# Kernel tuning notes

Hardware: AMD Instinct MI355X
Metric: run time of the kernel (lower is better)

## Reference

```python
import jax, jax.numpy as jnp
import numpy as np

L, V, D, H, F, S = 6, 32000, 768, 12, 3072, 1024
B, T = 2, 1024
DK = D // H
EPS = 1e-5  # torch LayerNorm default


def _ln(x, w, b):
    m = x.mean(-1, keepdims=True)
    v = ((x - m) ** 2).mean(-1, keepdims=True)
    return (x - m) / jnp.sqrt(v + EPS) * w + b


def setup_inputs() -> dict:
    key = jax.random.key(0)
    ks = jax.random.split(key, 16)
    n = lambda k, shape: jax.random.normal(k, shape, jnp.float32) * 0.02
    return {
        "x": jax.random.randint(ks[0], (B, T), 0, V),
        "tok_emb": n(ks[1], (V, D)),
        "pos_emb": n(ks[2], (S, D)),
        "ln1_w": jnp.ones((L, D), jnp.float32), "ln1_b": jnp.zeros((L, D), jnp.float32),
        "wq": n(ks[3], (L, D, D)), "bq": jnp.zeros((L, D), jnp.float32),
        "wk": n(ks[4], (L, D, D)), "bk": jnp.zeros((L, D), jnp.float32),
        "wv": n(ks[5], (L, D, D)), "bv": jnp.zeros((L, D), jnp.float32),
        "wo": n(ks[6], (L, D, D)), "bo": jnp.zeros((L, D), jnp.float32),
        "ln2_w": jnp.ones((L, D), jnp.float32), "ln2_b": jnp.zeros((L, D), jnp.float32),
        "w1": n(ks[7], (L, F, D)), "b1": jnp.zeros((L, F), jnp.float32),
        "w2": n(ks[8], (L, D, F)), "b2": jnp.zeros((L, D), jnp.float32),
        "lnf_w": jnp.ones((D,), jnp.float32), "lnf_b": jnp.zeros((D,), jnp.float32),
        "head_w": n(ks[9], (V, D)),
    }


def reference(x, tok_emb, pos_emb, ln1_w, ln1_b, wq, bq, wk, bk, wv, bv, wo, bo,
              ln2_w, ln2_b, w1, b1, w2, b2, lnf_w, lnf_b, head_w):
    Bx, Tx = x.shape
    h = tok_emb[x] + pos_emb[:Tx]                     # [B,T,D]
    causal = jnp.triu(jnp.ones((Tx, Tx), bool), 1)    # True above diagonal
    scale = 1.0 / np.sqrt(DK)
    for i in range(L):
        a = _ln(h, ln1_w[i], ln1_b[i])
        q = (a @ wq[i].T + bq[i]).reshape(Bx, Tx, H, DK).transpose(0, 2, 1, 3)
        k = (a @ wk[i].T + bk[i]).reshape(Bx, Tx, H, DK).transpose(0, 2, 1, 3)
        v = (a @ wv[i].T + bv[i]).reshape(Bx, Tx, H, DK).transpose(0, 2, 1, 3)
        scores = jnp.einsum("bhtd,bhsd->bhts", q, k) * scale  # [B,H,T,T]
        scores = jnp.where(causal, -jnp.inf, scores)
        attn = jax.nn.softmax(scores, axis=-1)
        ctx = jnp.einsum("bhts,bhsd->bhtd", attn, v)
        ctx = ctx.transpose(0, 2, 1, 3).reshape(Bx, Tx, D)
        h = h + ctx @ wo[i].T + bo[i]
        f = _ln(h, ln2_w[i], ln2_b[i])
        h = h + jax.nn.relu(f @ w1[i].T + b1[i]) @ w2[i].T + b2[i]
    h = _ln(h, lnf_w, lnf_b)
    return h @ head_w.T                               # [B,T,V] logits
```

## Files before the change

### kernel.cpp

```cpp
#include <hip/hip_runtime.h>

typedef unsigned short u16;
typedef __bf16 bf16x8 __attribute__((ext_vector_type(8)));
typedef float f32x4 __attribute__((ext_vector_type(4)));
typedef float f32x4v __attribute__((ext_vector_type(4)));
typedef u16 u16x4 __attribute__((ext_vector_type(4)));

__device__ __forceinline__ float bf2f(u16 u) {
    unsigned x = ((unsigned)u) << 16;
    return __builtin_bit_cast(float, x);
}
__device__ __forceinline__ u16 f2bf(float f) {
    unsigned x = __builtin_bit_cast(unsigned, f);
    unsigned r = (x + 0x7FFFu + ((x >> 16) & 1u)) >> 16;
    return (u16)r;
}

__global__ __launch_bounds__(256) void cvt_kernel(const float* __restrict__ in,
                                                  u16* __restrict__ out, long n) {
    for (long i = (long)blockIdx.x * 1024 + (long)threadIdx.x * 4; i < n;
         i += (long)gridDim.x * 1024) {
        f32x4v v = *(const f32x4v*)(in + i);
        u16x4 o;
        o.x = f2bf(v.x); o.y = f2bf(v.y); o.z = f2bf(v.z); o.w = f2bf(v.w);
        *(u16x4*)(out + i) = o;
    }
}

__global__ __launch_bounds__(256) void bias_fuse_kernel(const float* __restrict__ bq,
                                                        const float* __restrict__ bk,
                                                        const float* __restrict__ bv,
                                                        float* __restrict__ dst) {
    int i = blockIdx.x * 256 + threadIdx.x;
    if (i < 6 * 768) {
        int l = i / 768, j = i % 768;
        dst[l * 2304 + j] = bq[i];
        dst[l * 2304 + 768 + j] = bk[i];
        dst[l * 2304 + 1536 + j] = bv[i];
    }
}

__global__ __launch_bounds__(256) void embed_kernel(const int* __restrict__ x,
                                                    const float* __restrict__ tok,
                                                    const float* __restrict__ pos,
                                                    float* __restrict__ h) {
    int row = blockIdx.x;
    int t = row & 1023;
    long id = x[row];
    const float* te = tok + id * 768L;
    const float* pe = pos + (long)t * 768L;
    float* o = h + (long)row * 768L;
    for (int d = threadIdx.x; d < 768; d += 256) o[d] = te[d] + pe[d];
}

__global__ __launch_bounds__(256) void ln_kernel(const float* __restrict__ x,
                                                 const float* __restrict__ w,
                                                 const float* __restrict__ b,
                                                 u16* __restrict__ out) {
    __shared__ float red[4];
    int row = blockIdx.x;
    const float* xr = x + (long)row * 768L;
    int tid = threadIdx.x, lane = tid & 63, wid = tid >> 6;
    float v0 = xr[tid], v1 = xr[tid + 256], v2 = xr[tid + 512];
    float s = v0 + v1 + v2;
    for (int o = 32; o; o >>= 1) s += __shfl_xor(s, o);
    if (lane == 0) red[wid] = s;
    __syncthreads();
    float mean = (red[0] + red[1] + red[2] + red[3]) * (1.f / 768.f);
    __syncthreads();
    float d0 = v0 - mean, d1 = v1 - mean, d2 = v2 - mean;
    float q = d0 * d0 + d1 * d1 + d2 * d2;
    for (int o = 32; o; o >>= 1) q += __shfl_xor(q, o);
    if (lane == 0) red[wid] = q;
    __syncthreads();
    float var = (red[0] + red[1] + red[2] + red[3]) * (1.f / 768.f);
    float rstd = rsqrtf(var + 1e-5f);
    u16* orow = out + (long)row * 768L;
    orow[tid]       = f2bf(d0 * rstd * w[tid]       + b[tid]);
    orow[tid + 256] = f2bf(d1 * rstd * w[tid + 256] + b[tid + 256]);
    orow[tid + 512] = f2bf(d2 * rstd * w[tid + 512] + b[tid + 512]);
}

__global__ __launch_bounds__(256) void redln_kernel(
    const float* __restrict__ part, long pstride, int S,
    const float* __restrict__ bias, float* __restrict__ h,
    const float* __restrict__ w, const float* __restrict__ b,
    u16* __restrict__ out) {
    __shared__ float red[4];
    int row = blockIdx.x;
    int tid = threadIdx.x, lane = tid & 63, wid = tid >> 6;
    long base = (long)row * 768;
    float v[3];
#pragma unroll
    for (int e3 = 0; e3 < 3; e3++) {
        int e = tid + 256 * e3;
        float x = h[base + e] + bias[e];
        for (int s = 0; s < S; s++) x += part[(long)s * pstride + base + e];
        v[e3] = x;
        h[base + e] = x;
    }
    float s = v[0] + v[1] + v[2];
    for (int o = 32; o; o >>= 1) s += __shfl_xor(s, o);
    if (lane == 0) red[wid] = s;
    __syncthreads();
    float mean = (red[0] + red[1] + red[2] + red[3]) * (1.f / 768.f);
    __syncthreads();
    float d0 = v[0] - mean, d1 = v[1] - mean, d2 = v[2] - mean;
    float q = d0 * d0 + d1 * d1 + d2 * d2;
    for (int o = 32; o; o >>= 1) q += __shfl_xor(q, o);
    if (lane == 0) red[wid] = q;
    __syncthreads();
    float var = (red[0] + red[1] + red[2] + red[3]) * (1.f / 768.f);
    float rstd = rsqrtf(var + 1e-5f);
    u16* orow = out + base;
    orow[tid]       = f2bf(d0 * rstd * w[tid]       + b[tid]);
    orow[tid + 256] = f2bf(d1 * rstd * w[tid + 256] + b[tid + 256]);
    orow[tid + 512] = f2bf(d2 * rstd * w[tid + 512] + b[tid + 512]);
}

__global__ __launch_bounds__(256) void flash_kernel(
    const u16* __restrict__ qkv,
    const u16* __restrict__ vT,
    u16* __restrict__ ctx) {
    int z = blockIdx.z;
    int zb = z / 12, zh = z - zb * 12;
    int qt = (int)gridDim.x - 1 - (int)blockIdx.x;
    int q0 = qt * 64;
    int tid = threadIdx.x, lane = tid & 63, wid = tid >> 6;
    int rA = lane & 15, sA = lane >> 4;

    const u16* Qbase = qkv + (long)zb * 1024 * 2304 + zh * 64;
    const u16* Kbase = Qbase + 768;
    const u16* Vbase = vT + (long)z * 64 * 1024;

    __shared__ u16 Ks[64 * 64];
    __shared__ u16 Vs[64 * 64];
    __shared__ u16 Ps[4][16 * 64];

    bf16x8 aq[2];
    {
        const u16* qrow = Qbase + (long)(q0 + wid * 16 + rA) * 2304;
        aq[0] = *(const bf16x8*)(qrow + sA * 8);
        aq[1] = *(const bf16x8*)(qrow + 32 + sA * 8);
    }

    float m[4], l[4];
    f32x4 acc_o[4];
#pragma unroll
    for (int j = 0; j < 4; j++) { m[j] = -1e30f; l[j] = 0.f; }
#pragma unroll
    for (int nf = 0; nf < 4; nf++) acc_o[nf] = 0.f;

    int grow0 = q0 + wid * 16 + sA * 4;
    int nkv = qt + 1;
    for (int t = 0; t < nkv; ++t) {
        int kv0 = t * 64;
#pragma unroll
        for (int c0 = 0; c0 < 512; c0 += 256) {
            int c = c0 + tid;
            int row = c >> 3, half = (c >> 2) & 1, sl = c & 3;
            int ks = sl ^ ((row >> 1) & 3);
            __builtin_amdgcn_global_load_lds(
                (const __attribute__((address_space(1))) unsigned*)(Kbase + (long)(kv0 + row) * 2304 + half * 32 + ks * 8),
                (__attribute__((address_space(3))) unsigned*)(Ks + c * 8), 16, 0, 0);
        }
#pragma unroll
        for (int c0 = 0; c0 < 512; c0 += 256) {
            int c = c0 + tid;
            int row = c >> 3, half = (c >> 2) & 1, sl = c & 3;
            int ks = sl ^ ((row >> 1) & 3);
            __builtin_amdgcn_global_load_lds(
                (const __attribute__((address_space(1))) unsigned*)(Vbase + (long)row * 1024 + kv0 + half * 32 + ks * 8),
                (__attribute__((address_space(3))) unsigned*)(Vs + c * 8), 16, 0, 0);
        }
        __syncthreads();

        f32x4 s[4];
#pragma unroll
        for (int nf = 0; nf < 4; nf++) s[nf] = 0.f;
#pragma unroll
        for (int h = 0; h < 2; h++)
#pragma unroll
            for (int nf = 0; nf < 4; nf++) {
                int row = nf * 16 + rA;
                bf16x8 bk_ = *(const bf16x8*)(Ks + row * 64 + h * 32 + ((sA ^ ((row >> 1) & 3))) * 8);
                s[nf] = __builtin_amdgcn_mfma_f32_16x16x32_bf16(aq[h], bk_, s[nf], 0, 0, 0);
            }
#pragma unroll
        for (int nf = 0; nf < 4; nf++) {
            int col = kv0 + nf * 16 + rA;
#pragma unroll
            for (int j = 0; j < 4; j++)
                s[nf][j] = (col <= grow0 + j) ? s[nf][j] * 0.125f : -1e30f;
        }
        float pm[4];
#pragma unroll
        for (int j = 0; j < 4; j++) {
            float v = fmaxf(fmaxf(s[0][j], s[1][j]), fmaxf(s[2][j], s[3][j]));
#pragma unroll
            for (int o = 1; o < 16; o <<= 1) v = fmaxf(v, __shfl_xor(v, o));
            pm[j] = v;
        }
        float esc[4];
#pragma unroll
        for (int j = 0; j < 4; j++) {
            float mn = fmaxf(m[j], pm[j]);
            esc[j] = __expf(m[j] - mn);
            m[j] = mn;
        }
        float ts[4] = {0.f, 0.f, 0.f, 0.f};
#pragma unroll
        for (int nf = 0; nf < 4; nf++) {
            int c = nf * 16 + rA;
            int half = c >> 5, ch = (c >> 3) & 3, e = c & 7;
#pragma unroll
            for (int j = 0; j < 4; j++) {
                float p = __expf(s[nf][j] - m[j]);
                ts[j] += p;
                int r = sA * 4 + j;
                Ps[wid][r * 64 + half * 32 + (ch ^ ((r >> 1) & 3)) * 8 + e] = f2bf(p);
            }
        }
#pragma unroll
        for (int j = 0; j < 4; j++) {
            float v = ts[j];
#pragma unroll
            for (int o = 1; o < 16; o <<= 1) v += __shfl_xor(v, o);
            l[j] = l[j] * esc[j] + v;
        }
#pragma unroll
        for (int nf = 0; nf < 4; nf++)
#pragma unroll
            for (int j = 0; j < 4; j++) acc_o[nf][j] *= esc[j];

#pragma unroll
        for (int h = 0; h < 2; h++) {
            bf16x8 ap = *(const bf16x8*)(Ps[wid] + rA * 64 + h * 32 + ((sA ^ ((rA >> 1) & 3))) * 8);
#pragma unroll
            for (int nf = 0; nf < 4; nf++) {
                int row = nf * 16 + rA;
                bf16x8 bv_ = *(const bf16x8*)(Vs + row * 64 + h * 32 + ((sA ^ ((row >> 1) & 3))) * 8);
                acc_o[nf] = __builtin_amdgcn_mfma_f32_16x16x32_bf16(ap, bv_, acc_o[nf], 0, 0, 0);
            }
        }
        __syncthreads();
    }

    float inv[4];
#pragma unroll
    for (int j = 0; j < 4; j++) inv[j] = 1.f / l[j];
    u16* crow = ctx + ((long)zb * 1024 + q0 + wid * 16) * 768 + zh * 64;
#pragma unroll
    for (int nf = 0; nf < 4; nf++)
#pragma unroll
        for (int j = 0; j < 4; j++)
            crow[(long)(sA * 4 + j) * 768 + nf * 16 + rA] = f2bf(acc_o[nf][j] * inv[j]);
}

template <int BM, int BN, int EPI, int SK>
__global__ __launch_bounds__(256) void gemm3_kernel(
    const u16* __restrict__ A, int lda,
    const u16* __restrict__ Bm, int ldb,
    void* __restrict__ Cv, int ldc,
    const float* __restrict__ bias, int Kslice, int gm,
    u16* __restrict__ aux, int gemmBlocks, long partStride,
    const float* __restrict__ c0src, u16* __restrict__ c0dst, long c0n,
    const float* __restrict__ c1src, u16* __restrict__ c1dst, long c1n) {
    constexpr int BK = 32;
    int flat = blockIdx.x;
    int tid = threadIdx.x;
    if (flat >= gemmBlocks) {
        int P = (int)gridDim.x - gemmBlocks;
        int pid = flat - gemmBlocks;
        int P0 = P >> 1;
        const float* src; u16* dst; long n; long b0; long nb;
        if (pid < P0) { src = c0src; dst = c0dst; n = c0n; b0 = pid; nb = P0; }
        else { src = c1src; dst = c1dst; n = c1n; b0 = pid - P0; nb = P - P0; }
        if (src) {
            for (long i = b0 * 1024 + (long)tid * 4; i < n; i += nb * 1024) {
                f32x4v v = *(const f32x4v*)(src + i);
                u16x4 o;
                o.x = f2bf(v.x); o.y = f2bf(v.y); o.z = f2bf(v.z); o.w = f2bf(v.w);
                *(u16x4*)(dst + i) = o;
            }
        }
        return;
    }
    int nwg = gemmBlocks;
    int qq = nwg >> 3, rr = nwg & 7;
    int xcd = flat & 7, wi = flat >> 3;
    int swz = (xcd < rr) ? (xcd * (qq + 1) + wi) : (rr * (qq + 1) + (xcd - rr) * qq + wi);
    int slice = 0, wblk = swz;
    if (SK > 1) { int nbs = nwg / SK; slice = swz / nbs; wblk = swz - slice * nbs; }
    int ntile = wblk / gm, mt = wblk - ntile * gm;
    int bm0 = mt * BM, bn0 = ntile * BN;
    long koff = (long)slice * Kslice;
    const u16* Ab = A + (long)bm0 * lda + koff;
    const u16* Bb = Bm + (long)bn0 * ldb + koff;

    __shared__ u16 As[2][BM * BK];
    __shared__ u16 Bs[2][BN * BK];

    int lane = tid & 63, wid = tid >> 6;
    constexpr int WM = BM / 2, WN = BN / 2, MR = WM / 16, NR = WN / 16;
    int wm0 = (wid >> 1) * WM, wn0 = (wid & 1) * WN;

    f32x4 acc[MR][NR];
#pragma unroll
    for (int mi = 0; mi < MR; mi++)
#pragma unroll
        for (int ni = 0; ni < NR; ni++) acc[mi][ni] = 0.f;

    int nt = Kslice / BK;

    auto stage = [&](int buf, int k0) {
        constexpr int CA = BM * 4;
#pragma unroll
        for (int c0 = 0; c0 < CA; c0 += 256) {
            int c = c0 + tid;
            int row = c >> 2, sl = c & 3;
            int ks = sl ^ ((row >> 1) & 3);
            __builtin_amdgcn_global_load_lds(
                (const __attribute__((address_space(1))) unsigned*)(Ab + (long)row * lda + k0 + ks * 8),
                (__attribute__((address_space(3))) unsigned*)(As[buf] + c * 8), 16, 0, 0);
        }
        constexpr int CB = BN * 4;
#pragma unroll
        for (int c0 = 0; c0 < CB; c0 += 256) {
            int c = c0 + tid;
            int row = c >> 2, sl = c & 3;
            int ks = sl ^ ((row >> 1) & 3);
            __builtin_amdgcn_global_load_lds(
                (const __attribute__((address_space(1))) unsigned*)(Bb + (long)row * ldb + k0 + ks * 8),
                (__attribute__((address_space(3))) unsigned*)(Bs[buf] + c * 8), 16, 0, 0);
        }
    };

    stage(0, 0);
    __syncthreads();
    int cur = 0;
    int rA = lane & 15, sA = lane >> 4;
    int sswz = (sA ^ ((rA >> 1) & 3)) * 8;
    for (int t = 0; t < nt; ++t) {
        if (t + 1 < nt) stage(cur ^ 1, (t + 1) * BK);
        bf16x8 af[MR], bfr[NR];
#pragma unroll
        for (int mi = 0; mi < MR; mi++)
            af[mi] = *(const bf16x8*)(As[cur] + (wm0 + mi * 16 + rA) * BK + sswz);
#pragma unroll
        for (int ni = 0; ni < NR; ni++)
            bfr[ni] = *(const bf16x8*)(Bs[cur] + (wn0 + ni * 16 + rA) * BK + sswz);
#pragma unroll
        for (int mi = 0; mi < MR; mi++)
#pragma unroll
            for (int ni = 0; ni < NR; ni++)
                acc[mi][ni] = __builtin_amdgcn_mfma_f32_16x16x32_bf16(
                    af[mi], bfr[ni], acc[mi][ni], 0, 0, 0);
        __syncthreads();
        cur ^= 1;
    }

#pragma unroll
    for (int mi = 0; mi < MR; mi++)
#pragma unroll
        for (int ni = 0; ni < NR; ni++) {
            int gmb = bm0 + wm0 + mi * 16 + ((lane >> 4) << 2);
            int gn = bn0 + wn0 + ni * 16 + (lane & 15);
            if (EPI == 6) {
                if (gn < 1536) {
#pragma unroll
                    for (int j = 0; j < 4; j++)
                        ((u16*)Cv)[(long)(gmb + j) * ldc + gn] =
                            f2bf(acc[mi][ni][j] + bias[gn]);
                } else {
                    u16x4 o;
#pragma unroll
                    for (int j = 0; j < 4; j++) o[j] = f2bf(acc[mi][ni][j] + bias[gn]);
                    int hh = (gn - 1536) >> 6, dk = gn & 63;
                    long off = ((long)((gmb >> 10) * 12 + hh) * 64 + dk) * 1024 + (gmb & 1023);
                    *(u16x4*)(aux + off) = o;
                }
            } else {
#pragma unroll
                for (int j = 0; j < 4; j++) {
                    float v = acc[mi][ni][j];
                    long idx = (long)(gmb + j) * ldc + gn;
                    if (EPI == 2) ((u16*)Cv)[idx] = f2bf(fmaxf(v + bias[gn], 0.f));
                    else ((float*)Cv)[(long)slice * partStride + idx] = v;
                }
            }
        }
}

extern "C" void kernel_launch(void* const* d_in, const int* in_sizes, int n_in,
                              void* d_out, int out_size, void* d_ws, size_t ws_size,
                              hipStream_t stream) {
    const int L = 6, D = 768, F = 3072, T = 1024, V = 32000;
    const int M = 2048;
    const int* x = (const int*)d_in[0];
    const float* tok = (const float*)d_in[1];
    const float* pos = (const float*)d_in[2];
    const float* ln1w = (const float*)d_in[3];
    const float* ln1b = (const float*)d_in[4];
    const float* wq = (const float*)d_in[5];
    const float* bq = (const float*)d_in[6];
    const float* wk = (const float*)d_in[7];
    const float* bk = (const float*)d_in[8];
    const float* wv = (const float*)d_in[9];
    const float* bv = (const float*)d_in[10];
    const float* wo = (const float*)d_in[11];
    const float* bo = (const float*)d_in[12];
    const float* ln2w = (const float*)d_in[13];
    const float* ln2b = (const float*)d_in[14];
    const float* w1 = (const float*)d_in[15];
    const float* b1 = (const float*)d_in[16];
    const float* w2 = (const float*)d_in[17];
    const float* b2 = (const float*)d_in[18];
    const float* lnfw = (const float*)d_in[19];
    const float* lnfb = (const float*)d_in[20];
    const float* headw = (const float*)d_in[21];

    char* p = (char*)d_ws;
    auto alloc = [&](size_t bytes) {
        char* r = p;
        p += (bytes + 255) & ~(size_t)255;
        return r;
    };
    const long DD = (long)D * D, FD = (long)F * D;
    const long PS = (long)M * D;
    const long HC = 2048000;
    u16* qkvw_b = (u16*)alloc(L * 3 * DD * 2);
    u16* wo_b = (u16*)alloc(L * DD * 2);
    u16* w1_b = (u16*)alloc(L * FD * 2);
    u16* w2_b = (u16*)alloc(L * FD * 2);
    u16* hw_b = (u16*)alloc((long)V * D * 2);
    float* qkvbias = (float*)alloc(L * 2304 * 4);
    float* h = (float*)alloc((long)M * D * 4);
    u16* a = (u16*)alloc((long)M * D * 2);
    u16* qkvb = (u16*)alloc((long)M * 2304 * 2);
    u16* vT = (u16*)alloc(24L * 64 * T * 2);
    u16* ctxb = (u16*)alloc((long)M * D * 2);
    u16* f1 = (u16*)alloc((long)M * F * 2);
    float* part = (float*)alloc(4L * PS * 4);

    auto cvt = [&](const float* src, u16* dst, long n) {
        long blocks = (n + 1023) / 1024;
        if (blocks > 4096) blocks = 4096;
        cvt_kernel<<<dim3((unsigned)blocks), 256, 0, stream>>>(src, dst, n);
    };
    cvt(wq, qkvw_b, DD);
    cvt(wk, qkvw_b + DD, DD);
    cvt(wv, qkvw_b + 2 * DD, DD);
    cvt(wo, wo_b, DD);
    cvt(w1, w1_b, FD);
    cvt(w2, w2_b, FD);
    bias_fuse_kernel<<<dim3(18), 256, 0, stream>>>(bq, bk, bv, qkvbias);
    embed_kernel<<<dim3(M), 256, 0, stream>>>(x, tok, pos, h);
    ln_kernel<<<dim3(M), 256, 0, stream>>>(h, ln1w, ln1b, a);

    for (int i = 0; i < L; i++) {
        int nx = i + 1;
        bool hn = nx < L;
        {
            int pg = hn ? 128 : 0;
            gemm3_kernel<128, 128, 6, 1><<<dim3(288 + pg), 256, 0, stream>>>(
                a, D, qkvw_b + i * 3 * DD, D, qkvb, 2304, qkvbias + i * 2304,
                D, 16, vT, 288, 0,
                hn ? wq + nx * DD : nullptr, qkvw_b + nx * 3 * DD, DD,
                hn ? wk + nx * DD : nullptr, qkvw_b + nx * 3 * DD + DD, DD);
        }
        flash_kernel<<<dim3(16, 1, 24), 256, 0, stream>>>(qkvb, vT, ctxb);
        gemm3_kernel<64, 128, 5, 2><<<dim3(384 + 128), 256, 0, stream>>>(
            ctxb, D, wo_b + i * DD, D, part, D, nullptr, 384, 32, nullptr,
            384, PS,
            hn ? wv + nx * DD : nullptr, qkvw_b + nx * 3 * DD + 2 * DD, DD,
            hn ? wo + nx * DD : nullptr, wo_b + nx * DD, DD);
        redln_kernel<<<dim3(M), 256, 0, stream>>>(
            part, PS, 2, bo + i * D, h, ln2w + i * D, ln2b + i * D, a);
        gemm3_kernel<128, 128, 2, 1><<<dim3(384 + 128), 256, 0, stream>>>(
            a, D, w1_b + i * FD, D, f1, F, b1 + i * F, D, 16, nullptr, 384, 0,
            hn ? w1 + nx * FD : nullptr, w1_b + nx * FD, FD,
            headw + (2 * i) * HC, hw_b + (2 * i) * HC, HC);
        gemm3_kernel<64, 128, 5, 4><<<dim3(768 + 128), 256, 0, stream>>>(
            f1, F, w2_b + i * FD, F, part, D, nullptr, 768, 32, nullptr,
            768, PS,
            hn ? w2 + nx * FD : nullptr, w2_b + nx * FD, FD,
            headw + (2 * i + 1) * HC, hw_b + (2 * i + 1) * HC, HC);
        redln_kernel<<<dim3(M), 256, 0, stream>>>(
            part, PS, 4, b2 + i * D, h,
            hn ? ln1w + nx * D : lnfw, hn ? ln1b + nx * D : lnfb, a);
    }
    gemm3_kernel<128, 128, 5, 1><<<dim3(4000), 256, 0, stream>>>(
        a, D, hw_b, D, d_out, V, nullptr, D, 16, nullptr, 4000, 0,
        nullptr, nullptr, 0, nullptr, nullptr, 0);
}
```

Measured before the change: 1.114 ms.

## Load GEMM fragments directly from global into registers instead of LDS staging

Drops the LDS double-buffered staging in the GEMM kernel. Each wave now loads its MFMA fragments straight from global memory into registers, with a two-deep register prefetch, and the per-tile __syncthreads is removed. This cuts the LDS round trip and the barriers, but gives up sharing data between waves, so each operand row is fetched by several waves (relying on L1/L2) and the global loads are less coalesced. The fp32-to-bf16 conversion loops also process 8 elements per thread instead of 4.

```diff
diff --git a/kernel.cpp b/kernel.cpp
--- a/kernel.cpp
+++ b/kernel.cpp
@@ -18,12 +18,15 @@
 
 __global__ __launch_bounds__(256) void cvt_kernel(const float* __restrict__ in,
                                                   u16* __restrict__ out, long n) {
-    for (long i = (long)blockIdx.x * 1024 + (long)threadIdx.x * 4; i < n;
-         i += (long)gridDim.x * 1024) {
-        f32x4v v = *(const f32x4v*)(in + i);
-        u16x4 o;
-        o.x = f2bf(v.x); o.y = f2bf(v.y); o.z = f2bf(v.z); o.w = f2bf(v.w);
-        *(u16x4*)(out + i) = o;
+    for (long i = (long)blockIdx.x * 2048 + (long)threadIdx.x * 8; i < n;
+         i += (long)gridDim.x * 2048) {
+        f32x4v v0 = *(const f32x4v*)(in + i);
+        f32x4v v1 = *(const f32x4v*)(in + i + 4);
+        u16x4 o0, o1;
+        o0.x = f2bf(v0.x); o0.y = f2bf(v0.y); o0.z = f2bf(v0.z); o0.w = f2bf(v0.w);
+        o1.x = f2bf(v1.x); o1.y = f2bf(v1.y); o1.z = f2bf(v1.z); o1.w = f2bf(v1.w);
+        *(u16x4*)(out + i) = o0;
+        *(u16x4*)(out + i + 4) = o1;
     }
 }
 
@@ -258,7 +261,7 @@
 }
 
 template <int BM, int BN, int EPI, int SK>
-__global__ __launch_bounds__(256) void gemm3_kernel(
+__global__ __launch_bounds__(256) void gemm6_kernel(
     const u16* __restrict__ A, int lda,
     const u16* __restrict__ Bm, int ldb,
     void* __restrict__ Cv, int ldc,
@@ -277,11 +280,14 @@
         if (pid < P0) { src = c0src; dst = c0dst; n = c0n; b0 = pid; nb = P0; }
         else { src = c1src; dst = c1dst; n = c1n; b0 = pid - P0; nb = P - P0; }
         if (src) {
-            for (long i = b0 * 1024 + (long)tid * 4; i < n; i += nb * 1024) {
-                f32x4v v = *(const f32x4v*)(src + i);
-                u16x4 o;
-                o.x = f2bf(v.x); o.y = f2bf(v.y); o.z = f2bf(v.z); o.w = f2bf(v.w);
-                *(u16x4*)(dst + i) = o;
+            for (long i = b0 * 2048 + (long)tid * 8; i < n; i += nb * 2048) {
+                f32x4v v0 = *(const f32x4v*)(src + i);
+                f32x4v v1 = *(const f32x4v*)(src + i + 4);
+                u16x4 o0, o1;
+                o0.x = f2bf(v0.x); o0.y = f2bf(v0.y); o0.z = f2bf(v0.z); o0.w = f2bf(v0.w);
+                o1.x = f2bf(v1.x); o1.y = f2bf(v1.y); o1.z = f2bf(v1.z); o1.w = f2bf(v1.w);
+                *(u16x4*)(dst + i) = o0;
+                *(u16x4*)(dst + i + 4) = o1;
             }
         }
         return;
@@ -295,15 +301,20 @@
     int ntile = wblk / gm, mt = wblk - ntile * gm;
     int bm0 = mt * BM, bn0 = ntile * BN;
     long koff = (long)slice * Kslice;
-    const u16* Ab = A + (long)bm0 * lda + koff;
-    const u16* Bb = Bm + (long)bn0 * ldb + koff;
-
-    __shared__ u16 As[2][BM * BK];
-    __shared__ u16 Bs[2][BN * BK];
 
     int lane = tid & 63, wid = tid >> 6;
     constexpr int WM = BM / 2, WN = BN / 2, MR = WM / 16, NR = WN / 16;
     int wm0 = (wid >> 1) * WM, wn0 = (wid & 1) * WN;
+    int rA = lane & 15, sA = lane >> 4;
+
+    const u16* ap[MR];
+    const u16* bp[NR];
+#pragma unroll
+    for (int mi = 0; mi < MR; mi++)
+        ap[mi] = A + (long)(bm0 + wm0 + mi * 16 + rA) * lda + koff + sA * 8;
+#pragma unroll
+    for (int ni = 0; ni < NR; ni++)
+        bp[ni] = Bm + (long)(bn0 + wn0 + ni * 16 + rA) * ldb + koff + sA * 8;
 
     f32x4 acc[MR][NR];
 #pragma unroll
@@ -313,51 +324,36 @@
 
     int nt = Kslice / BK;
 
-    auto stage = [&](int buf, int k0) {
-        constexpr int CA = BM * 4;
-#pragma unroll
-        for (int c0 = 0; c0 < CA; c0 += 256) {
-            int c = c0 + tid;
-            int row = c >> 2, sl = c & 3;
-            int ks = sl ^ ((row >> 1) & 3);
-            __builtin_amdgcn_global_load_lds(
-                (const __attribute__((address_space(1))) unsigned*)(Ab + (long)row * lda + k0 + ks * 8),
-                (__attribute__((address_space(3))) unsigned*)(As[buf] + c * 8), 16, 0, 0);
-        }
-        constexpr int CB = BN * 4;
-#pragma unroll
-        for (int c0 = 0; c0 < CB; c0 += 256) {
-            int c = c0 + tid;
-            int row = c >> 2, sl = c & 3;
-            int ks = sl ^ ((row >> 1) & 3);
-            __builtin_amdgcn_global_load_lds(
-                (const __attribute__((address_space(1))) unsigned*)(Bb + (long)row * ldb + k0 + ks * 8),
-                (__attribute__((address_space(3))) unsigned*)(Bs[buf] + c * 8), 16, 0, 0);
-        }
-    };
-
-    stage(0, 0);
-    __syncthreads();
-    int cur = 0;
-    int rA = lane & 15, sA = lane >> 4;
-    int sswz = (sA ^ ((rA >> 1) & 3)) * 8;
-    for (int t = 0; t < nt; ++t) {
-        if (t + 1 < nt) stage(cur ^ 1, (t + 1) * BK);
-        bf16x8 af[MR], bfr[NR];
-#pragma unroll
-        for (int mi = 0; mi < MR; mi++)
-            af[mi] = *(const bf16x8*)(As[cur] + (wm0 + mi * 16 + rA) * BK + sswz);
-#pragma unroll
-        for (int ni = 0; ni < NR; ni++)
-            bfr[ni] = *(const bf16x8*)(Bs[cur] + (wn0 + ni * 16 + rA) * BK + sswz);
+    bf16x8 a0[MR], b0[NR], a1[MR], b1[NR];
+#pragma unroll
+    for (int mi = 0; mi < MR; mi++) a0[mi] = *(const bf16x8*)(ap[mi]);
+#pragma unroll
+    for (int ni = 0; ni < NR; ni++) b0[ni] = *(const bf16x8*)(bp[ni]);
+
+    for (int i = 0; i < nt / 2; ++i) {
+        int t1 = 2 * i + 1, t2 = 2 * i + 2;
+#pragma unroll
+        for (int mi = 0; mi < MR; mi++) a1[mi] = *(const bf16x8*)(ap[mi] + t1 * BK);
+#pragma unroll
+        for (int ni = 0; ni < NR; ni++) b1[ni] = *(const bf16x8*)(bp[ni] + t1 * BK);
 #pragma unroll
         for (int mi = 0; mi < MR; mi++)
 #pragma unroll
             for (int ni = 0; ni < NR; ni++)
                 acc[mi][ni] = __builtin_amdgcn_mfma_f32_16x16x32_bf16(
-                    af[mi], bfr[ni], acc[mi][ni], 0, 0, 0);
-        __syncthreads();
-        cur ^= 1;
+                    a0[mi], b0[ni], acc[mi][ni], 0, 0, 0);
+        if (t2 < nt) {
+#pragma unroll
+            for (int mi = 0; mi < MR; mi++) a0[mi] = *(const bf16x8*)(ap[mi] + t2 * BK);
+#pragma unroll
+            for (int ni = 0; ni < NR; ni++) b0[ni] = *(const bf16x8*)(bp[ni] + t2 * BK);
+        }
+#pragma unroll
+        for (int mi = 0; mi < MR; mi++)
+#pragma unroll
+            for (int ni = 0; ni < NR; ni++)
+                acc[mi][ni] = __builtin_amdgcn_mfma_f32_16x16x32_bf16(
+                    a1[mi], b1[ni], acc[mi][ni], 0, 0, 0);
     }
 
 #pragma unroll
@@ -444,7 +440,7 @@
     float* part = (float*)alloc(4L * PS * 4);
 
     auto cvt = [&](const float* src, u16* dst, long n) {
-        long blocks = (n + 1023) / 1024;
+        long blocks = (n + 2047) / 2048;
         if (blocks > 4096) blocks = 4096;
         cvt_kernel<<<dim3((unsigned)blocks), 256, 0, stream>>>(src, dst, n);
     };
@@ -463,25 +459,25 @@
         bool hn = nx < L;
         {
             int pg = hn ? 128 : 0;
-            gemm3_kernel<128, 128, 6, 1><<<dim3(288 + pg), 256, 0, stream>>>(
+            gemm6_kernel<128, 128, 6, 1><<<dim3(288 + pg), 256, 0, stream>>>(
                 a, D, qkvw_b + i * 3 * DD, D, qkvb, 2304, qkvbias + i * 2304,
                 D, 16, vT, 288, 0,
                 hn ? wq + nx * DD : nullptr, qkvw_b + nx * 3 * DD, DD,
                 hn ? wk + nx * DD : nullptr, qkvw_b + nx * 3 * DD + DD, DD);
         }
         flash_kernel<<<dim3(16, 1, 24), 256, 0, stream>>>(qkvb, vT, ctxb);
-        gemm3_kernel<64, 128, 5, 2><<<dim3(384 + 128), 256, 0, stream>>>(
+        gemm6_kernel<64, 128, 5, 2><<<dim3(384 + 128), 256, 0, stream>>>(
             ctxb, D, wo_b + i * DD, D, part, D, nullptr, 384, 32, nullptr,
             384, PS,
             hn ? wv + nx * DD : nullptr, qkvw_b + nx * 3 * DD + 2 * DD, DD,
             hn ? wo + nx * DD : nullptr, wo_b + nx * DD, DD);
         redln_kernel<<<dim3(M), 256, 0, stream>>>(
             part, PS, 2, bo + i * D, h, ln2w + i * D, ln2b + i * D, a);
-        gemm3_kernel<128, 128, 2, 1><<<dim3(384 + 128), 256, 0, stream>>>(
+        gemm6_kernel<128, 128, 2, 1><<<dim3(384 + 128), 256, 0, stream>>>(
             a, D, w1_b + i * FD, D, f1, F, b1 + i * F, D, 16, nullptr, 384, 0,
             hn ? w1 + nx * FD : nullptr, w1_b + nx * FD, FD,
             headw + (2 * i) * HC, hw_b + (2 * i) * HC, HC);
-        gemm3_kernel<64, 128, 5, 4><<<dim3(768 + 128), 256, 0, stream>>>(
+        gemm6_kernel<64, 128, 5, 4><<<dim3(768 + 128), 256, 0, stream>>>(
             f1, F, w2_b + i * FD, F, part, D, nullptr, 768, 32, nullptr,
             768, PS,
             hn ? w2 + nx * FD : nullptr, w2_b + nx * FD, FD,
@@ -490,7 +486,7 @@
             part, PS, 4, b2 + i * D, h,
             hn ? ln1w + nx * D : lnfw, hn ? ln1b + nx * D : lnfb, a);
     }
-    gemm3_kernel<128, 128, 5, 1><<<dim3(4000), 256, 0, stream>>>(
+    gemm6_kernel<128, 128, 5, 1><<<dim3(4000), 256, 0, stream>>>(
         a, D, hw_b, D, d_out, V, nullptr, D, 16, nullptr, 4000, 0,
         nullptr, nullptr, 0, nullptr, nullptr, 0);
 }
```

Result: slower. 1.808 ms (+62.3%).

## Load GEMM A-operand directly to registers and add MFMA priority hints in flash

Applied to the files above, without the earlier changes.

The GEMM kernel stops staging the A tile through LDS. Each wave now loads its A fragments straight from global memory into registers, double-buffered across an unrolled two-step K loop, while B stays staged in LDS via global_load_lds. The aim is to cut LDS traffic and LDS footprint for A. The cost is that A rows are read redundantly by the two waves sharing them, with less coalesced global loads. The flash attention kernel also wraps its MFMA sections in s_setprio to favour matrix issue; the unrolled GEMM loop assumes an even tile count.

```diff
diff --git a/kernel.cpp b/kernel.cpp
--- a/kernel.cpp
+++ b/kernel.cpp
@@ -178,6 +178,7 @@
         f32x4 s[4];
 #pragma unroll
         for (int nf = 0; nf < 4; nf++) s[nf] = 0.f;
+        __builtin_amdgcn_s_setprio(1);
 #pragma unroll
         for (int h = 0; h < 2; h++)
 #pragma unroll
@@ -186,6 +187,7 @@
                 bf16x8 bk_ = *(const bf16x8*)(Ks + row * 64 + h * 32 + ((sA ^ ((row >> 1) & 3))) * 8);
                 s[nf] = __builtin_amdgcn_mfma_f32_16x16x32_bf16(aq[h], bk_, s[nf], 0, 0, 0);
             }
+        __builtin_amdgcn_s_setprio(0);
 #pragma unroll
         for (int nf = 0; nf < 4; nf++) {
             int col = kv0 + nf * 16 + rA;
@@ -233,6 +235,7 @@
 #pragma unroll
             for (int j = 0; j < 4; j++) acc_o[nf][j] *= esc[j];
 
+        __builtin_amdgcn_s_setprio(1);
 #pragma unroll
         for (int h = 0; h < 2; h++) {
             bf16x8 ap = *(const bf16x8*)(Ps[wid] + rA * 64 + h * 32 + ((sA ^ ((rA >> 1) & 3))) * 8);
@@ -243,6 +246,7 @@
                 acc_o[nf] = __builtin_amdgcn_mfma_f32_16x16x32_bf16(ap, bv_, acc_o[nf], 0, 0, 0);
             }
         }
+        __builtin_amdgcn_s_setprio(0);
         __syncthreads();
     }
 
@@ -258,7 +262,7 @@
 }
 
 template <int BM, int BN, int EPI, int SK>
-__global__ __launch_bounds__(256) void gemm3_kernel(
+__global__ __launch_bounds__(256) void gemm7_kernel(
     const u16* __restrict__ A, int lda,
     const u16* __restrict__ Bm, int ldb,
     void* __restrict__ Cv, int ldc,
@@ -295,15 +299,19 @@
     int ntile = wblk / gm, mt = wblk - ntile * gm;
     int bm0 = mt * BM, bn0 = ntile * BN;
     long koff = (long)slice * Kslice;
-    const u16* Ab = A + (long)bm0 * lda + koff;
     const u16* Bb = Bm + (long)bn0 * ldb + koff;
 
-    __shared__ u16 As[2][BM * BK];
     __shared__ u16 Bs[2][BN * BK];
 
     int lane = tid & 63, wid = tid >> 6;
     constexpr int WM = BM / 2, WN = BN / 2, MR = WM / 16, NR = WN / 16;
     int wm0 = (wid >> 1) * WM, wn0 = (wid & 1) * WN;
+    int rA = lane & 15, sA = lane >> 4;
+
+    const u16* ap[MR];
+#pragma unroll
+    for (int mi = 0; mi < MR; mi++)
+        ap[mi] = A + (long)(bm0 + wm0 + mi * 16 + rA) * lda + koff + sA * 8;
 
     f32x4 acc[MR][NR];
 #pragma unroll
@@ -313,17 +321,7 @@
 
     int nt = Kslice / BK;
 
-    auto stage = [&](int buf, int k0) {
-        constexpr int CA = BM * 4;
-#pragma unroll
-        for (int c0 = 0; c0 < CA; c0 += 256) {
-            int c = c0 + tid;
-            int row = c >> 2, sl = c & 3;
-            int ks = sl ^ ((row >> 1) & 3);
-            __builtin_amdgcn_global_load_lds(
-                (const __attribute__((address_space(1))) unsigned*)(Ab + (long)row * lda + k0 + ks * 8),
-                (__attribute__((address_space(3))) unsigned*)(As[buf] + c * 8), 16, 0, 0);
-        }
+    auto stageB = [&](int buf, int k0) {
         constexpr int CB = BN * 4;
 #pragma unroll
         for (int c0 = 0; c0 < CB; c0 += 256) {
@@ -336,28 +334,50 @@
         }
     };
 
-    stage(0, 0);
-    __syncthreads();
-    int cur = 0;
-    int rA = lane & 15, sA = lane >> 4;
     int sswz = (sA ^ ((rA >> 1) & 3)) * 8;
-    for (int t = 0; t < nt; ++t) {
-        if (t + 1 < nt) stage(cur ^ 1, (t + 1) * BK);
-        bf16x8 af[MR], bfr[NR];
-#pragma unroll
-        for (int mi = 0; mi < MR; mi++)
-            af[mi] = *(const bf16x8*)(As[cur] + (wm0 + mi * 16 + rA) * BK + sswz);
-#pragma unroll
-        for (int ni = 0; ni < NR; ni++)
-            bfr[ni] = *(const bf16x8*)(Bs[cur] + (wn0 + ni * 16 + rA) * BK + sswz);
-#pragma unroll
-        for (int mi = 0; mi < MR; mi++)
+
+    bf16x8 a0[MR], a1[MR];
+#pragma unroll
+    for (int mi = 0; mi < MR; mi++) a0[mi] = *(const bf16x8*)(ap[mi]);
+    stageB(0, 0);
+    __syncthreads();
+
+    for (int i = 0; i < nt / 2; ++i) {
+        int t1 = 2 * i + 1, t2 = 2 * i + 2;
+        stageB(1, t1 * BK);
+#pragma unroll
+        for (int mi = 0; mi < MR; mi++) a1[mi] = *(const bf16x8*)(ap[mi] + t1 * BK);
+        {
+            bf16x8 bfr[NR];
 #pragma unroll
             for (int ni = 0; ni < NR; ni++)
-                acc[mi][ni] = __builtin_amdgcn_mfma_f32_16x16x32_bf16(
-                    af[mi], bfr[ni], acc[mi][ni], 0, 0, 0);
+                bfr[ni] = *(const bf16x8*)(Bs[0] + (wn0 + ni * 16 + rA) * BK + sswz);
+#pragma unroll
+            for (int mi = 0; mi < MR; mi++)
+#pragma unroll
+                for (int ni = 0; ni < NR; ni++)
+                    acc[mi][ni] = __builtin_amdgcn_mfma_f32_16x16x32_bf16(
+                        a0[mi], bfr[ni], acc[mi][ni], 0, 0, 0);
+        }
         __syncthreads();
-        cur ^= 1;
+        if (t2 < nt) {
+            stageB(0, t2 * BK);
+#pragma unroll
+            for (int mi = 0; mi < MR; mi++) a0[mi] = *(const bf16x8*)(ap[mi] + t2 * BK);
+        }
+        {
+            bf16x8 bfr[NR];
+#pragma unroll
+            for (int ni = 0; ni < NR; ni++)
+                bfr[ni] = *(const bf16x8*)(Bs[1] + (wn0 + ni * 16 + rA) * BK + sswz);
+#pragma unroll
+            for (int mi = 0; mi < MR; mi++)
+#pragma unroll
+                for (int ni = 0; ni < NR; ni++)
+                    acc[mi][ni] = __builtin_amdgcn_mfma_f32_16x16x32_bf16(
+                        a1[mi], bfr[ni], acc[mi][ni], 0, 0, 0);
+        }
+        __syncthreads();
     }
 
 #pragma unroll
@@ -463,25 +483,25 @@
         bool hn = nx < L;
         {
             int pg = hn ? 128 : 0;
-            gemm3_kernel<128, 128, 6, 1><<<dim3(288 + pg), 256, 0, stream>>>(
+            gemm7_kernel<128, 128, 6, 1><<<dim3(288 + pg), 256, 0, stream>>>(
                 a, D, qkvw_b + i * 3 * DD, D, qkvb, 2304, qkvbias + i * 2304,
                 D, 16, vT, 288, 0,
                 hn ? wq + nx * DD : nullptr, qkvw_b + nx * 3 * DD, DD,
                 hn ? wk + nx * DD : nullptr, qkvw_b + nx * 3 * DD + DD, DD);
         }
         flash_kernel<<<dim3(16, 1, 24), 256, 0, stream>>>(qkvb, vT, ctxb);
-        gemm3_kernel<64, 128, 5, 2><<<dim3(384 + 128), 256, 0, stream>>>(
+        gemm7_kernel<64, 128, 5, 2><<<dim3(384 + 128), 256, 0, stream>>>(
             ctxb, D, wo_b + i * DD, D, part, D, nullptr, 384, 32, nullptr,
             384, PS,
             hn ? wv + nx * DD : nullptr, qkvw_b + nx * 3 * DD + 2 * DD, DD,
             hn ? wo + nx * DD : nullptr, wo_b + nx * DD, DD);
         redln_kernel<<<dim3(M), 256, 0, stream>>>(
             part, PS, 2, bo + i * D, h, ln2w + i * D, ln2b + i * D, a);
-        gemm3_kernel<128, 128, 2, 1><<<dim3(384 + 128), 256, 0, stream>>>(
+        gemm7_kernel<128, 128, 2, 1><<<dim3(384 + 128), 256, 0, stream>>>(
             a, D, w1_b + i * FD, D, f1, F, b1 + i * F, D, 16, nullptr, 384, 0,
             hn ? w1 + nx * FD : nullptr, w1_b + nx * FD, FD,
             headw + (2 * i) * HC, hw_b + (2 * i) * HC, HC);
-        gemm3_kernel<64, 128, 5, 4><<<dim3(768 + 128), 256, 0, stream>>>(
+        gemm7_kernel<64, 128, 5, 4><<<dim3(768 + 128), 256, 0, stream>>>(
             f1, F, w2_b + i * FD, F, part, D, nullptr, 768, 32, nullptr,
             768, PS,
             hn ? w2 + nx * FD : nullptr, w2_b + nx * FD, FD,
@@ -490,7 +510,7 @@
             part, PS, 4, b2 + i * D, h,
             hn ? ln1w + nx * D : lnfw, hn ? ln1b + nx * D : lnfb, a);
     }
-    gemm3_kernel<128, 128, 5, 1><<<dim3(4000), 256, 0, stream>>>(
+    gemm7_kernel<128, 128, 5, 1><<<dim3(4000), 256, 0, stream>>>(
         a, D, hw_b, D, d_out, V, nullptr, D, 16, nullptr, 4000, 0,
         nullptr, nullptr, 0, nullptr, nullptr, 0);
 }
```

Result: slower. 1.342 ms (+20.4%).
